# Performance work log

Measured on AMD Instinct MI355X. Metric: run time of the kernel, lower is better.

Reference implementation:

```python
import jax, jax.numpy as jnp
import numpy as np

LAYERS = 2      # LightGCN propagation layers
LAMB = 0.5      # aux loss weight
REG = 1e-4      # embedding reg weight
N_AUX = 2       # len(behaviors) - 1


def setup_inputs() -> dict:
    key = jax.random.key(0)
    k = jax.random.split(key, 8)
    n_users, n_items, d = 100000, 50000, 32
    E = 1000000
    user_emb = (jax.random.normal(k[0], (n_users + 1, d), jnp.float32) * 0.1).at[0].set(0.0)
    item_emb = (jax.random.normal(k[1], (n_items + 1, d), jnp.float32) * 0.1).at[0].set(0.0)
    aux_u = jax.random.randint(k[2], (N_AUX, E), 1, n_users + 1)
    aux_i = jax.random.randint(k[3], (N_AUX, E), 1, n_items + 1)
    aux_edges = jnp.stack([aux_u, aux_i], axis=-1).astype(jnp.int32)
    tgt_u = jax.random.randint(k[4], (E,), 1, n_users + 1)
    tgt_i = jax.random.randint(k[5], (E,), 1, n_items + 1)
    target_edges = jnp.stack([tgt_u, tgt_i], axis=-1).astype(jnp.int32)
    # [B, 1+N_AUX, 3]: per row (user, pos_item, neg_item) for target then each aux behavior
    batch_data = jax.random.randint(k[6], (4096, 1 + N_AUX, 3), 1, n_items + 1).astype(jnp.int32)
    return {"user_emb": user_emb, "item_emb": item_emb, "batch_data": batch_data,
            "aux_edges": aux_edges, "target_edges": target_edges}


def _graph(edges, n_user_rows, N):
    """Symmetric-normalized bipartite LightGCN graph as directed COO (src, dst, w)."""
    u = edges[:, 0]
    v = edges[:, 1] + n_user_rows  # shift item ids into joint node space
    ones = jnp.ones(u.shape[0], jnp.float32)
    deg = jax.ops.segment_sum(ones, u, num_segments=N) + jax.ops.segment_sum(ones, v, num_segments=N)
    dinv = jnp.where(deg > 0, jax.lax.rsqrt(jnp.maximum(deg, 1.0)), 0.0)
    w = dinv[u] * dinv[v]
    src = jnp.concatenate([u, v])
    dst = jnp.concatenate([v, u])
    w2 = jnp.concatenate([w, w])
    return src, dst, w2


def _lightgcn(emb, src, dst, w, N):
    """L-layer LightGCN propagation, mean over layers 0..L."""
    acc = emb
    cur = emb
    for _ in range(LAYERS):
        cur = jax.ops.segment_sum(w[:, None] * cur[src], dst, num_segments=N)
        acc = acc + cur
    return acc / (LAYERS + 1)


def _prob(ue, ie, u, i):
    return jax.nn.relu(jnp.sum(ue[u] * ie[i], axis=-1))


def _bpr(p, n):
    return -jnp.mean(jax.nn.log_sigmoid(p - n))


def reference(user_emb, item_emb, batch_data, aux_edges, target_edges):
    Nu = user_emb.shape[0]
    N = Nu + item_emb.shape[0]
    all_emb = jnp.concatenate([user_emb, item_emb], axis=0)
    tgt_g = _graph(target_edges, Nu, N)

    user, p_item, n_item = batch_data[:, 0, 0], batch_data[:, 0, 1], batch_data[:, 0, 2]
    aux_user, aux_p, aux_n = batch_data[:, 1:, 0], batch_data[:, 1:, 1], batch_data[:, 1:, 2]

    cps, cns, dps, dns, aps, ans, aux_losses = [], [], [], [], [], [], []
    for idx in range(N_AUX):
        # combine graph = aux behavior edges union target edges
        comb_edges = jnp.concatenate([aux_edges[idx], target_edges], axis=0)
        ce = _lightgcn(all_emb, *_graph(comb_edges, Nu, N), N)
        cu, ci = ce[:Nu], ce[Nu:]
        cps.append(_prob(cu, ci, user, p_item))
        cns.append(_prob(cu, ci, user, n_item))

        ae = _lightgcn(all_emb, *_graph(aux_edges[idx], Nu, N), N)
        au, ai = ae[:Nu], ae[Nu:]
        aps.append(_prob(au, ai, user, p_item))
        ans.append(_prob(au, ai, user, n_item))

        # condition: propagate aux embeddings through the target graph
        de = _lightgcn(ae, *tgt_g, N)
        du, di = de[:Nu], de[Nu:]
        dps.append(_prob(du, di, user, p_item))
        dns.append(_prob(du, di, user, n_item))

        ps = jnp.sum(au[aux_user[:, idx]] * ai[aux_p[:, idx]], axis=-1)
        ns = jnp.sum(au[aux_user[:, idx]] * ai[aux_n[:, idx]], axis=-1)
        aux_losses.append(_bpr(ps, ns))

    aux_loss = jnp.mean(jnp.stack(aux_losses))

    def front_door(cond, comb, aux):
        return jnp.sum(cond * jnp.sum(comb * aux, axis=0), axis=0)

    p_scores = front_door(jnp.stack(dps), jnp.stack(cps), jnp.stack(aps))
    n_scores = front_door(jnp.stack(dns), jnp.stack(cns), jnp.stack(ans))
    rec_loss = _bpr(p_scores, n_scores)
    emb_loss = (jnp.linalg.norm(user_emb) + jnp.linalg.norm(item_emb)) / item_emb.shape[0]
    return rec_loss + LAMB * aux_loss + REG * emb_loss
```

## Files before the change

### kernel.cpp

```cpp
#include <hip/hip_runtime.h>
#include <math.h>

#define D 32
#define ROWU 16
#define NBK 1024
#define BSHIFT 8
#define TILE_H 16384
#define TILE_BIN 2048
#define BCAP 7680

typedef unsigned int u32;
typedef unsigned short u16;

__device__ __forceinline__ float logsigf(float x) {
  return fminf(x, 0.f) - log1pf(expf(-fabsf(x)));
}

__device__ __forceinline__ float lo16(u32 u) { return __uint_as_float(u << 16); }
__device__ __forceinline__ float hi16(u32 u) { return __uint_as_float(u & 0xFFFF0000u); }
__device__ __forceinline__ u32 pk2(float a, float b) {
  u32 ua = __float_as_uint(a), ub = __float_as_uint(b);
  u32 ra = (ua + 0x7FFFu + ((ua >> 16) & 1u)) >> 16;
  u32 rb = (ub + 0x7FFFu + ((ub >> 16) & 1u)) >> 16;
  return (ra & 0xFFFFu) | (rb << 16);
}
__device__ __forceinline__ float bfat(const u16* __restrict__ p, size_t off) {
  return __uint_as_float(((u32)p[off]) << 16);
}
__device__ __forceinline__ void accum8(float* a, float w, uint4 x) {
  a[0] += w * lo16(x.x); a[1] += w * hi16(x.x);
  a[2] += w * lo16(x.y); a[3] += w * hi16(x.y);
  a[4] += w * lo16(x.z); a[5] += w * hi16(x.z);
  a[6] += w * lo16(x.w); a[7] += w * hi16(x.w);
}
__device__ __forceinline__ uint4 pack8(const float* a, float w) {
  return make_uint4(pk2(w * a[0], w * a[1]), pk2(w * a[2], w * a[3]),
                    pk2(w * a[4], w * a[5]), pk2(w * a[6], w * a[7]));
}


__global__ void hist_kernel(const int2* __restrict__ tgt, const int2* __restrict__ aux,
                            int E, int Nu, int BPS, int* __restrict__ bcur) {
  __shared__ int lh[NBK];
  int seg = blockIdx.x / BPS;
  int blk = blockIdx.x - seg * BPS;
  const int2* edges = (seg == 0) ? tgt : aux + (size_t)(seg - 1) * E;
  for (int b = threadIdx.x; b < NBK; b += 256) lh[b] = 0;
  __syncthreads();
  int e0 = blk * TILE_H;
  for (int k = threadIdx.x; k < TILE_H; k += 256) {
    int e = e0 + k;
    if (e < E) {
      int2 ed = edges[e];
      atomicAdd(&lh[ed.x >> BSHIFT], 1);
      atomicAdd(&lh[(ed.y + Nu) >> BSHIFT], 1);
    }
  }
  __syncthreads();
  for (int b = threadIdx.x; b < NBK; b += 256)
    if (lh[b]) atomicAdd(&bcur[seg * NBK + b], lh[b]);
}

__global__ void bscan_kernel(int* __restrict__ bcur) {
  int* b = bcur + blockIdx.x * NBK;
  int lane = threadIdx.x;
  int carry = 0;
  for (int base = 0; base < NBK; base += 64) {
    int i = base + lane;
    int v = b[i];
    int s = v;
    #pragma unroll
    for (int o = 1; o < 64; o <<= 1) {
      int t = __shfl_up(s, o);
      if (lane >= o) s += t;
    }
    b[i] = carry + s - v;
    carry += __shfl(s, 63);
  }
}

__global__ void bin_kernel(const int2* __restrict__ tgt, const int2* __restrict__ aux,
                           int E, int Nu, int BPS, int* __restrict__ bcur,
                           int* __restrict__ binned) {
  __shared__ int stage[2 * TILE_BIN];
  __shared__ int lh[NBK];
  __shared__ int loff[NBK];
  __shared__ int gb[NBK];
  __shared__ int wred[4];
  __shared__ int stot;
  int seg = blockIdx.x / BPS;
  int blk = blockIdx.x - seg * BPS;
  const int2* edges = (seg == 0) ? tgt : aux + (size_t)(seg - 1) * E;
  int* out = binned + (size_t)seg * 2 * E;
  int tid = threadIdx.x;
  for (int b = tid; b < NBK; b += 256) lh[b] = 0;
  __syncthreads();
  int e0 = blk * TILE_BIN;
  int pkv[16];
  int pb[16];
  int pr[16];
  #pragma unroll
  for (int it = 0; it < 8; ++it) {
    int e = e0 + tid + it * 256;
    bool ok = e < E;
    int2 ed = ok ? edges[e] : make_int2(0, -Nu);
    int u = ed.x, v = ed.y + Nu;
    int b1 = u >> BSHIFT, b2 = v >> BSHIFT;
    pkv[2 * it] = ((u & 255) << 18) | v;
    pb[2 * it] = b1;
    pr[2 * it] = ok ? atomicAdd(&lh[b1], 1) : 0;
    pkv[2 * it + 1] = ((v & 255) << 18) | u;
    pb[2 * it + 1] = b2;
    pr[2 * it + 1] = ok ? atomicAdd(&lh[b2], 1) : 0;
  }
  __syncthreads();
  int lane = tid & 63, wid = tid >> 6;
  int b4 = tid * 4;
  int v0 = lh[b4], v1 = lh[b4 + 1], v2 = lh[b4 + 2], v3 = lh[b4 + 3];
  int tsum = v0 + v1 + v2 + v3;
  int incl = tsum;
  #pragma unroll
  for (int o = 1; o < 64; o <<= 1) {
    int t = __shfl_up(incl, o);
    if (lane >= o) incl += t;
  }
  if (lane == 63) wred[wid] = incl;
  __syncthreads();
  int wbase = 0;
  for (int w = 0; w < wid; ++w) wbase += wred[w];
  int excl = wbase + incl - tsum;
  loff[b4] = excl;
  loff[b4 + 1] = excl + v0;
  loff[b4 + 2] = excl + v0 + v1;
  loff[b4 + 3] = excl + v0 + v1 + v2;
  if (tid == 255) stot = excl + tsum;
  #pragma unroll
  for (int j = 0; j < 4; ++j) {
    int b = b4 + j;
    int c = lh[b];
    gb[b] = c ? atomicAdd(&bcur[seg * NBK + b], c) : 0;
  }
  __syncthreads();
  #pragma unroll
  for (int it = 0; it < 16; ++it) {
    int e = e0 + tid + (it >> 1) * 256;
    if (e < E) stage[loff[pb[it]] + pr[it]] = pkv[it];
  }
  __syncthreads();
  int tot = stot;
  for (int k = tid; k < tot; k += 256) {
    int lo = 0, hi = NBK;
    while (lo < hi) {
      int mid = (lo + hi) >> 1;
      if (loff[mid] <= k) lo = mid + 1; else hi = mid;
    }
    int b = lo - 1;
    out[gb[b] + (k - loff[b])] = stage[k];
  }
}

__global__ void bucket_csr_kernel(const int* __restrict__ binned,
                                  const int* __restrict__ bend, int E2, int N, int NBKe,
                                  int* __restrict__ deg3, int* __restrict__ rp3,
                                  int* __restrict__ col_all) {
  __shared__ int ent[BCAP];
  __shared__ int cnt[256];
  __shared__ int off[256];
  __shared__ int wred[4];
  int seg = blockIdx.x / NBKe;
  int bkt = blockIdx.x - seg * NBKe;
  int node0 = bkt << BSHIFT;
  const int* bc = bend + seg * NBK;
  int start = (bkt == 0) ? 0 : bc[bkt - 1];
  int end = bc[bkt];
  int cntE = end - start;
  const int* src = binned + (size_t)seg * E2 + start;
  bool inLds = (cntE <= BCAP);
  if (inLds)
    for (int k = threadIdx.x; k < cntE; k += 256) ent[k] = src[k];
  cnt[threadIdx.x] = 0;
  __syncthreads();
  for (int k = threadIdx.x; k < cntE; k += 256) {
    int en = inLds ? ent[k] : src[k];
    atomicAdd(&cnt[en >> 18], 1);
  }
  __syncthreads();
  int lane = threadIdx.x & 63, wid = threadIdx.x >> 6;
  int v = cnt[threadIdx.x];
  int incl = v;
  #pragma unroll
  for (int o = 1; o < 64; o <<= 1) {
    int t = __shfl_up(incl, o);
    if (lane >= o) incl += t;
  }
  if (lane == 63) wred[wid] = incl;
  __syncthreads();
  int wbase = 0;
  for (int w = 0; w < wid; ++w) wbase += wred[w];
  off[threadIdx.x] = wbase + incl - v;
  int node = node0 + (int)threadIdx.x;
  if (node < N) {
    deg3[(size_t)seg * N + node] = v;
    rp3[(size_t)seg * (N + 1) + node] = start + wbase + incl - v;
  }
  if (bkt == 0 && threadIdx.x == 0) rp3[(size_t)seg * (N + 1) + N] = E2;
  __syncthreads();
  cnt[threadIdx.x] = 0;
  __syncthreads();
  int* col = col_all + (size_t)seg * E2 + start;
  for (int k = threadIdx.x; k < cntE; k += 256) {
    int en = inLds ? ent[k] : src[k];
    int lb = en >> 18;
    int pos = atomicAdd(&cnt[lb], 1);
    col[off[lb] + pos] = en & 0x3FFFF;
  }
}

__global__ void dinv_all_kernel(const int* __restrict__ deg3, float* __restrict__ dinv5,
                                int N) {
  int n = blockIdx.x * blockDim.x + threadIdx.x;
  if (n >= N) return;
  int dt = deg3[n], d0 = deg3[N + n], d1 = deg3[2 * N + n];
  dinv5[n]         = dt ? rsqrtf((float)dt) : 0.f;
  dinv5[N + n]     = d0 ? rsqrtf((float)d0) : 0.f;
  dinv5[2 * N + n] = d1 ? rsqrtf((float)d1) : 0.f;
  int c0 = dt + d0, c1 = dt + d1;
  dinv5[3 * N + n] = c0 ? rsqrtf((float)c0) : 0.f;
  dinv5[4 * N + n] = c1 ? rsqrtf((float)c1) : 0.f;
}

__global__ void cvt_emb_kernel(const float2* __restrict__ ue, long nu2,
                               const float2* __restrict__ ie, long ni2,
                               u32* __restrict__ emb) {
  long i = (long)blockIdx.x * blockDim.x + threadIdx.x;
  if (i >= nu2 + ni2) return;
  float2 v = (i < nu2) ? ue[i] : ie[i - nu2];
  emb[i] = pk2(v.x, v.y);
}


__global__ void gather_fused_all_kernel(const int* __restrict__ rp3,
                                        const int* __restrict__ col_all,
                                        const float* __restrict__ dinv5,
                                        const uint4* __restrict__ emb,
                                        uint4* __restrict__ BaAll, uint4* __restrict__ BcAll,
                                        int N, int E2) {
  const int* rpA0 = rp3 + (size_t)1 * (N + 1);
  const int* rpA1 = rp3 + (size_t)2 * (N + 1);
  const int* colA0 = col_all + (size_t)1 * E2;
  const int* colA1 = col_all + (size_t)2 * E2;
  const float* dvA0 = dinv5 + (size_t)1 * N;
  const float* dvA1 = dinv5 + (size_t)2 * N;
  const float* dvC0 = dinv5 + (size_t)3 * N;
  const float* dvC1 = dinv5 + (size_t)4 * N;
  int t = blockIdx.x * blockDim.x + threadIdx.x;
  int n = t >> 2;
  if (n >= N) return;
  int lane = t & 3;
  float aA0[8] = {0, 0, 0, 0, 0, 0, 0, 0};
  float aA1[8] = {0, 0, 0, 0, 0, 0, 0, 0};
  float aC0[8] = {0, 0, 0, 0, 0, 0, 0, 0};
  float aC1[8] = {0, 0, 0, 0, 0, 0, 0, 0};
  int s = rpA0[n], e = rpA0[n + 1];
  int j = s;
  for (; j + 1 < e; j += 2) {
    int c0 = colA0[j], c1 = colA0[j + 1];
    float wa0 = dvA0[c0], wc0 = dvC0[c0];
    float wa1 = dvA0[c1], wc1 = dvC0[c1];
    uint4 x0 = emb[(size_t)c0 * 4 + lane];
    uint4 x1 = emb[(size_t)c1 * 4 + lane];
    accum8(aA0, wa0, x0); accum8(aC0, wc0, x0);
    accum8(aA0, wa1, x1); accum8(aC0, wc1, x1);
  }
  if (j < e) {
    int c = colA0[j];
    float wa = dvA0[c], wc = dvC0[c];
    uint4 x = emb[(size_t)c * 4 + lane];
    accum8(aA0, wa, x); accum8(aC0, wc, x);
  }
  s = rpA1[n]; e = rpA1[n + 1];
  j = s;
  for (; j + 1 < e; j += 2) {
    int c0 = colA1[j], c1 = colA1[j + 1];
    float wa0 = dvA1[c0], wc0 = dvC1[c0];
    float wa1 = dvA1[c1], wc1 = dvC1[c1];
    uint4 x0 = emb[(size_t)c0 * 4 + lane];
    uint4 x1 = emb[(size_t)c1 * 4 + lane];
    accum8(aA1, wa0, x0); accum8(aC1, wc0, x0);
    accum8(aA1, wa1, x1); accum8(aC1, wc1, x1);
  }
  if (j < e) {
    int c = colA1[j];
    float wa = dvA1[c], wc = dvC1[c];
    uint4 x = emb[(size_t)c * 4 + lane];
    accum8(aA1, wa, x); accum8(aC1, wc, x);
  }
  s = rp3[n]; e = rp3[n + 1];
  j = s;
  for (; j + 1 < e; j += 2) {
    int c0 = col_all[j], c1 = col_all[j + 1];
    float w00 = dvC0[c0], w10 = dvC1[c0];
    float w01 = dvC0[c1], w11 = dvC1[c1];
    uint4 x0 = emb[(size_t)c0 * 4 + lane];
    uint4 x1 = emb[(size_t)c1 * 4 + lane];
    accum8(aC0, w00, x0); accum8(aC1, w10, x0);
    accum8(aC0, w01, x1); accum8(aC1, w11, x1);
  }
  if (j < e) {
    int c = col_all[j];
    float w0 = dvC0[c], w1 = dvC1[c];
    uint4 x = emb[(size_t)c * 4 + lane];
    accum8(aC0, w0, x); accum8(aC1, w1, x);
  }
  size_t o = (size_t)n * 4 + lane;
  size_t rowN4 = (size_t)N * 4;
  BaAll[o] = pack8(aA0, dvA0[n]);
  BaAll[rowN4 + o] = pack8(aA1, dvA1[n]);
  BcAll[o] = pack8(aC0, dvC0[n]);
  BcAll[rowN4 + o] = pack8(aC1, dvC1[n]);
}

__global__ void gather_avg_kernel(const int* __restrict__ rp3, const int* __restrict__ col_all,
                                  const float* __restrict__ dinv5,
                                  const uint4* __restrict__ emb,
                                  const uint4* __restrict__ BaAll, uint4* __restrict__ AI,
                                  int N, int E2) {
  int idx = blockIdx.y;
  const int* rp = rp3 + (size_t)(1 + idx) * (N + 1);
  const int* col = col_all + (size_t)(1 + idx) * E2;
  const float* dv = dinv5 + (size_t)(1 + idx) * N;
  const uint4* cur = BaAll + (size_t)idx * N * 4;
  int t = blockIdx.x * blockDim.x + threadIdx.x;
  int n = t >> 2;
  if (n >= N) return;
  int lane = t & 3;
  float acc[8] = {0, 0, 0, 0, 0, 0, 0, 0};
  int s = rp[n], e = rp[n + 1];
  int j = s;
  for (; j + 3 < e; j += 4) {
    int c0 = col[j], c1 = col[j + 1], c2 = col[j + 2], c3 = col[j + 3];
    float w0 = dv[c0], w1 = dv[c1], w2 = dv[c2], w3 = dv[c3];
    uint4 x0 = cur[(size_t)c0 * 4 + lane];
    uint4 x1 = cur[(size_t)c1 * 4 + lane];
    uint4 x2 = cur[(size_t)c2 * 4 + lane];
    uint4 x3 = cur[(size_t)c3 * 4 + lane];
    accum8(acc, w0, x0);
    accum8(acc, w1, x1);
    accum8(acc, w2, x2);
    accum8(acc, w3, x3);
  }
  for (; j < e; ++j) {
    int c = col[j];
    float w = dv[c];
    uint4 x = cur[(size_t)c * 4 + lane];
    accum8(acc, w, x);
  }
  float wn = dv[n];
  uint4 e4 = emb[(size_t)n * 4 + lane];
  uint4 b4 = cur[(size_t)n * 4 + lane];
  float r[8];
  r[0] = (lo16(e4.x) + lo16(b4.x) + wn * acc[0]) * (1.f / 3.f);
  r[1] = (hi16(e4.x) + hi16(b4.x) + wn * acc[1]) * (1.f / 3.f);
  r[2] = (lo16(e4.y) + lo16(b4.y) + wn * acc[2]) * (1.f / 3.f);
  r[3] = (hi16(e4.y) + hi16(b4.y) + wn * acc[3]) * (1.f / 3.f);
  r[4] = (lo16(e4.z) + lo16(b4.z) + wn * acc[4]) * (1.f / 3.f);
  r[5] = (hi16(e4.z) + hi16(b4.z) + wn * acc[5]) * (1.f / 3.f);
  r[6] = (lo16(e4.w) + lo16(b4.w) + wn * acc[6]) * (1.f / 3.f);
  r[7] = (hi16(e4.w) + hi16(b4.w) + wn * acc[7]) * (1.f / 3.f);
  AI[(size_t)n * 8 + idx * 4 + lane] = pack8(r, 1.f);
}

__global__ void de_gather_kernel(const int* __restrict__ rp3, const int* __restrict__ col_all,
                                 const float* __restrict__ dinv5,
                                 const uint4* __restrict__ AI, uint4* __restrict__ DeI,
                                 int N) {
  int t = blockIdx.x * blockDim.x + threadIdx.x;
  int n = t >> 3;
  if (n >= N) return;
  int lane = t & 7;
  float acc[8] = {0, 0, 0, 0, 0, 0, 0, 0};
  int s = rp3[n], e = rp3[n + 1];
  int j = s;
  for (; j + 1 < e; j += 2) {
    int c0 = col_all[j], c1 = col_all[j + 1];
    float w0 = dinv5[c0], w1 = dinv5[c1];
    uint4 x0 = AI[(size_t)c0 * 8 + lane];
    uint4 x1 = AI[(size_t)c1 * 8 + lane];
    accum8(acc, w0, x0);
    accum8(acc, w1, x1);
  }
  if (j < e) {
    int c = col_all[j];
    float w = dinv5[c];
    uint4 x = AI[(size_t)c * 8 + lane];
    accum8(acc, w, x);
  }
  DeI[(size_t)n * 8 + lane] = pack8(acc, dinv5[n]);
}


__device__ __forceinline__ float fdim2(const int* __restrict__ rpA, const int* __restrict__ colA,
                                       const int* __restrict__ rpT, const int* __restrict__ colT,
                                       const float* __restrict__ dv,
                                       const u16* __restrict__ base, const u16* __restrict__ L1,
                                       int r, int d) {
  float acc = 0.f;
  for (int j = rpA[r]; j < rpA[r + 1]; ++j) {
    int c = colA[j];
    acc += dv[c] * bfat(L1, (size_t)c * D + d);
  }
  for (int j = rpT[r]; j < rpT[r + 1]; ++j) {
    int c = colT[j];
    acc += dv[c] * bfat(L1, (size_t)c * D + d);
  }
  return (bfat(base, (size_t)r * D + d) + bfat(L1, (size_t)r * D + d) + dv[r] * acc) * (1.f / 3.f);
}

__device__ __forceinline__ float fdim1i(const int* __restrict__ rp, const int* __restrict__ col,
                                        const float* __restrict__ dv,
                                        const u16* __restrict__ base, const u16* __restrict__ L1,
                                        int r, int di) {
  float acc = 0.f;
  for (int j = rp[r]; j < rp[r + 1]; ++j) {
    int c = col[j];
    acc += dv[c] * bfat(L1, (size_t)c * 64 + di);
  }
  return (bfat(base, (size_t)r * 64 + di) + bfat(L1, (size_t)r * 64 + di) + dv[r] * acc) * (1.f / 3.f);
}

__global__ void ce_sparse_kernel(const int* __restrict__ rp3, const int* __restrict__ col_all,
                                 const float* __restrict__ dinv5,
                                 const u32* __restrict__ EMBu, const u32* __restrict__ BcAll,
                                 const int* __restrict__ batch, int Bsz, int Nu, int N, int E2,
                                 float* __restrict__ cps, float* __restrict__ cns) {
  int idx = blockIdx.y;
  const int* rpA = rp3 + (size_t)(1 + idx) * (N + 1);
  const int* colA = col_all + (size_t)(1 + idx) * E2;
  const float* dv = dinv5 + (size_t)(3 + idx) * N;
  const u16* base = (const u16*)EMBu;
  const u16* L1 = (const u16*)(BcAll + (size_t)idx * N * ROWU);
  float* outp = cps + (size_t)idx * Bsz;
  float* outn = cns + (size_t)idx * Bsz;
  int t = blockIdx.x * blockDim.x + threadIdx.x;
  int b = t >> 5, d = t & 31;
  if (b >= Bsz) return;
  int u = batch[b * 9 + 0];
  int p = batch[b * 9 + 1] + Nu;
  int n = batch[b * 9 + 2] + Nu;
  float uv = fdim2(rpA, colA, rp3, col_all, dv, base, L1, u, d);
  float pv = fdim2(rpA, colA, rp3, col_all, dv, base, L1, p, d);
  float nv = fdim2(rpA, colA, rp3, col_all, dv, base, L1, n, d);
  float sp = uv * pv, sn = uv * nv;
  #pragma unroll
  for (int o = 16; o > 0; o >>= 1) {
    sp += __shfl_down(sp, o, 32);
    sn += __shfl_down(sn, o, 32);
  }
  if (d == 0) {
    outp[b] = fmaxf(sp, 0.f);
    outn[b] = fmaxf(sn, 0.f);
  }
}

__global__ void de_sparse_kernel(const int* __restrict__ rp3, const int* __restrict__ col_all,
                                 const float* __restrict__ dinv5,
                                 const u32* __restrict__ AI, const u32* __restrict__ DeI,
                                 const int* __restrict__ batch, int Bsz, int Nu, int N,
                                 float* __restrict__ dps, float* __restrict__ dns) {
  int idx = blockIdx.y;
  const u16* base = (const u16*)AI;
  const u16* L1 = (const u16*)DeI;
  float* outp = dps + (size_t)idx * Bsz;
  float* outn = dns + (size_t)idx * Bsz;
  int t = blockIdx.x * blockDim.x + threadIdx.x;
  int b = t >> 5, d = t & 31;
  if (b >= Bsz) return;
  int di = idx * 32 + d;
  int u = batch[b * 9 + 0];
  int p = batch[b * 9 + 1] + Nu;
  int n = batch[b * 9 + 2] + Nu;
  float uv = fdim1i(rp3, col_all, dinv5, base, L1, u, di);
  float pv = fdim1i(rp3, col_all, dinv5, base, L1, p, di);
  float nv = fdim1i(rp3, col_all, dinv5, base, L1, n, di);
  float sp = uv * pv, sn = uv * nv;
  #pragma unroll
  for (int o = 16; o > 0; o >>= 1) {
    sp += __shfl_down(sp, o, 32);
    sn += __shfl_down(sn, o, 32);
  }
  if (d == 0) {
    outp[b] = fmaxf(sp, 0.f);
    outn[b] = fmaxf(sn, 0.f);
  }
}


__device__ __forceinline__ float dotrow(const u32* __restrict__ a, const u32* __restrict__ b) {
  float s = 0.f;
  #pragma unroll
  for (int k = 0; k < ROWU; ++k) {
    u32 x = a[k], y = b[k];
    s += lo16(x) * lo16(y) + hi16(x) * hi16(y);
  }
  return s;
}

__global__ void score_aux_kernel(const u32* __restrict__ AI, const int* __restrict__ batch,
                                 int Bsz, int Nu, int N, float* __restrict__ aps,
                                 float* __restrict__ ans_, float* __restrict__ accs) {
  int idx = blockIdx.y;
  const u32* A = AI + (size_t)idx * ROWU;
  float* outp = aps + (size_t)idx * Bsz;
  float* outn = ans_ + (size_t)idx * Bsz;
  int b = blockIdx.x * blockDim.x + threadIdx.x;
  float l = 0.f;
  if (b < Bsz) {
    int u = batch[b * 9 + 0];
    int p = batch[b * 9 + 1] + Nu;
    int n = batch[b * 9 + 2] + Nu;
    const u32* ur = A + (size_t)u * 32;
    outp[b] = fmaxf(dotrow(ur, A + (size_t)p * 32), 0.f);
    outn[b] = fmaxf(dotrow(ur, A + (size_t)n * 32), 0.f);
    const int* r = batch + b * 9 + 3 * (1 + idx);
    const u32* aur = A + (size_t)r[0] * 32;
    float ps = dotrow(aur, A + (size_t)(r[1] + Nu) * 32);
    float ns = dotrow(aur, A + (size_t)(r[2] + Nu) * 32);
    l = -logsigf(ps - ns);
  }
  for (int o = 32; o > 0; o >>= 1) l += __shfl_down(l, o);
  if ((threadIdx.x & 63) == 0) atomicAdd(&accs[idx], l);
}

__global__ void recloss_kernel(const float* __restrict__ cps, const float* __restrict__ cns,
                               const float* __restrict__ aps, const float* __restrict__ ans_,
                               const float* __restrict__ dps, const float* __restrict__ dns,
                               int Bsz, int NA, float* __restrict__ acc) {
  int b = blockIdx.x * blockDim.x + threadIdx.x;
  float l = 0.f;
  if (b < Bsz) {
    float dp = 0.f, dn = 0.f, cap = 0.f, can = 0.f;
    for (int i = 0; i < NA; ++i) {
      dp += dps[i * Bsz + b];
      dn += dns[i * Bsz + b];
      cap += cps[i * Bsz + b] * aps[i * Bsz + b];
      can += cns[i * Bsz + b] * ans_[i * Bsz + b];
    }
    l = -logsigf(dp * cap - dn * can);
  }
  for (int o = 32; o > 0; o >>= 1) l += __shfl_down(l, o);
  if ((threadIdx.x & 63) == 0) atomicAdd(acc, l);
}

__global__ void sumsq2_kernel(const float4* __restrict__ xu, int n4u,
                              const float4* __restrict__ xi, int n4i,
                              float* __restrict__ accU, float* __restrict__ accI) {
  __shared__ float redU[4], redI[4];
  int tid = threadIdx.x;
  int gid = blockIdx.x * blockDim.x + tid;
  int stride = gridDim.x * blockDim.x;
  float su = 0.f, si = 0.f;
  for (int i = gid; i < n4u; i += stride) {
    float4 v = xu[i];
    su += v.x * v.x + v.y * v.y + v.z * v.z + v.w * v.w;
  }
  for (int i = gid; i < n4i; i += stride) {
    float4 v = xi[i];
    si += v.x * v.x + v.y * v.y + v.z * v.z + v.w * v.w;
  }
  for (int o = 32; o > 0; o >>= 1) {
    su += __shfl_down(su, o);
    si += __shfl_down(si, o);
  }
  if ((tid & 63) == 0) { redU[tid >> 6] = su; redI[tid >> 6] = si; }
  __syncthreads();
  if (tid == 0) {
    atomicAdd(accU, redU[0] + redU[1] + redU[2] + redU[3]);
    atomicAdd(accI, redI[0] + redI[1] + redI[2] + redI[3]);
  }
}

__global__ void final_kernel(const float* __restrict__ accs, int Bsz, int NA, int NiRows,
                             float* __restrict__ out) {
  float rec = accs[NA] / (float)Bsz;
  float aux = 0.f;
  for (int i = 0; i < NA; ++i) aux += accs[i] / (float)Bsz;
  aux /= (float)NA;
  float embl = (sqrtf(accs[NA + 1]) + sqrtf(accs[NA + 2])) / (float)NiRows;
  out[0] = rec + 0.5f * aux + 1e-4f * embl;
}

extern "C" void kernel_launch(void* const* d_in, const int* in_sizes, int n_in,
                              void* d_out, int out_size, void* d_ws, size_t ws_size,
                              hipStream_t stream) {
  const float* user_emb = (const float*)d_in[0];
  const float* item_emb = (const float*)d_in[1];
  const int* batch = (const int*)d_in[2];
  const int* aux_edges = (const int*)d_in[3];
  const int* tgt_edges = (const int*)d_in[4];

  const int NuRows = in_sizes[0] / D;
  const int NiRows = in_sizes[1] / D;
  const int Bsz = in_sizes[2] / 9;
  const int E = in_sizes[4] / 2;
  const int NA = in_sizes[3] / (2 * E);
  const int N = NuRows + NiRows;
  const int E2 = 2 * E;
  const size_t rowH = (size_t)N * ROWU;
  const int BPS_H = (E + TILE_H - 1) / TILE_H;
  const int BPS_B = (E + TILE_BIN - 1) / TILE_BIN;
  const int NBKe = (N + (1 << BSHIFT) - 1) >> BSHIFT;

  u32* EMBu = (u32*)d_ws;
  u32* AI = EMBu + rowH;
  u32* BaAll = AI + 2 * rowH;
  u32* BcAll = BaAll + 2 * rowH;
  int* deg3 = (int*)(BcAll + 2 * rowH);
  float* dinv5 = (float*)(deg3 + 3 * (size_t)N);
  int* rp3 = (int*)(dinv5 + 5 * (size_t)N);
  int* bcur = rp3 + 3 * (size_t)(N + 1);
  int* col_all = bcur + 3 * (size_t)NBK;
  float* cps = (float*)(col_all + 3 * (size_t)E2);
  float* cns = cps + (size_t)NA * Bsz;
  float* aps = cns + (size_t)NA * Bsz;
  float* ans_ = aps + (size_t)NA * Bsz;
  float* dps = ans_ + (size_t)NA * Bsz;
  float* dns = dps + (size_t)NA * Bsz;
  float* accs = dns + (size_t)NA * Bsz;
  int* binned = (int*)AI;

  const int TB = 256;
  const int gN = (N + TB - 1) / TB;
  const int gN4 = (N * 4 + TB - 1) / TB;
  const int gN8 = (N * 8 + TB - 1) / TB;
  const int gB = (Bsz + TB - 1) / TB;
  const int gB32 = (Bsz * 32 + TB - 1) / TB;
  const long nu2 = (long)NuRows * ROWU;
  const long ni2 = (long)NiRows * ROWU;
  const int gCvt = (int)((nu2 + ni2 + TB - 1) / TB);

  cvt_emb_kernel<<<gCvt, TB, 0, stream>>>((const float2*)user_emb, nu2,
                                          (const float2*)item_emb, ni2, EMBu);

  hipMemsetAsync(bcur, 0, 3 * (size_t)NBK * sizeof(int), stream);
  hist_kernel<<<3 * BPS_H, TB, 0, stream>>>((const int2*)tgt_edges, (const int2*)aux_edges,
                                            E, NuRows, BPS_H, bcur);
  bscan_kernel<<<3, 64, 0, stream>>>(bcur);
  bin_kernel<<<3 * BPS_B, TB, 0, stream>>>((const int2*)tgt_edges, (const int2*)aux_edges,
                                           E, NuRows, BPS_B, bcur, binned);
  bucket_csr_kernel<<<3 * NBKe, TB, 0, stream>>>(binned, bcur, E2, N, NBKe,
                                                 deg3, rp3, col_all);
  dinv_all_kernel<<<gN, TB, 0, stream>>>(deg3, dinv5, N);

  hipMemsetAsync(accs, 0, (size_t)(NA + 3) * sizeof(float), stream);

  dim3 gridG(gN4, NA), gridB(gB, NA), gridS(gB32, NA);

  gather_fused_all_kernel<<<gN4, TB, 0, stream>>>(rp3, col_all, dinv5, (const uint4*)EMBu,
                                                  (uint4*)BaAll, (uint4*)BcAll, N, E2);
  gather_avg_kernel<<<gridG, TB, 0, stream>>>(rp3, col_all, dinv5, (const uint4*)EMBu,
                                              (const uint4*)BaAll, (uint4*)AI, N, E2);
  score_aux_kernel<<<gridB, TB, 0, stream>>>(AI, batch, Bsz, NuRows, N, aps, ans_, accs);
  ce_sparse_kernel<<<gridS, TB, 0, stream>>>(rp3, col_all, dinv5, EMBu, BcAll,
                                             batch, Bsz, NuRows, N, E2, cps, cns);
  de_gather_kernel<<<gN8, TB, 0, stream>>>(rp3, col_all, dinv5, (const uint4*)AI,
                                           (uint4*)BaAll, N);
  de_sparse_kernel<<<gridS, TB, 0, stream>>>(rp3, col_all, dinv5, AI, BaAll,
                                             batch, Bsz, NuRows, N, dps, dns);

  sumsq2_kernel<<<104, TB, 0, stream>>>((const float4*)user_emb,
                                        (int)((size_t)NuRows * D / 4),
                                        (const float4*)item_emb,
                                        (int)((size_t)NiRows * D / 4),
                                        accs + NA + 1, accs + NA + 2);
  recloss_kernel<<<gB, TB, 0, stream>>>(cps, cns, aps, ans_, dps, dns, Bsz, NA, accs + NA);
  final_kernel<<<1, 1, 0, stream>>>(accs, Bsz, NA, NiRows, (float*)d_out);
}
```

Baseline: 651.1 us.

## Split CSR neighbor lists into column-range chunks for cache-local gathers

The CSR build now sorts each node's neighbors by column range (chunks of 2^15 nodes) and records the chunk boundaries in a new mids array. The gather kernels then loop over the chunks in the same order, so every node visits the same region of the embedding table at roughly the same time. The aim is better L2 locality for the random row gathers. In exchange there is more shared-memory and atomic work in bucket_csr, extra boundary loads and loop overhead per node, and more workspace. Threads can also drift apart, so the intended locality is only approximate.

Result: slower. 675.2 us (+3.7%).

```diff
diff --git a/kernel.cpp b/kernel.cpp
--- a/kernel.cpp
+++ b/kernel.cpp
@@ -8,6 +8,8 @@
 #define TILE_H 16384
 #define TILE_BIN 2048
 #define BCAP 7680
+#define RSH 15
+#define MAXR 8
 
 typedef unsigned int u32;
 typedef unsigned short u16;
@@ -36,6 +38,14 @@
 __device__ __forceinline__ uint4 pack8(const float* a, float w) {
   return make_uint4(pk2(w * a[0], w * a[1]), pk2(w * a[2], w * a[3]),
                     pk2(w * a[4], w * a[5]), pk2(w * a[6], w * a[7]));
+}
+
+__device__ __forceinline__ int2 rbounds(const int* __restrict__ rp,
+                                        const int* __restrict__ mids,
+                                        size_t segN, int n, int r, int nr) {
+  int b0 = (r == 0) ? rp[n] : mids[(segN + n) * (MAXR - 1) + (r - 1)];
+  int b1 = (r == nr - 1) ? rp[n + 1] : mids[(segN + n) * (MAXR - 1) + r];
+  return make_int2(b0, b1);
 }
 
 
@@ -161,11 +171,11 @@
 
 __global__ void bucket_csr_kernel(const int* __restrict__ binned,
                                   const int* __restrict__ bend, int E2, int N, int NBKe,
-                                  int* __restrict__ deg3, int* __restrict__ rp3,
-                                  int* __restrict__ col_all) {
+                                  int nr, int* __restrict__ deg3, int* __restrict__ rp3,
+                                  int* __restrict__ mids, int* __restrict__ col_all) {
   __shared__ int ent[BCAP];
-  __shared__ int cnt[256];
-  __shared__ int off[256];
+  __shared__ int cnt[256 * MAXR];
+  __shared__ int off[256 * MAXR];
   __shared__ int wred[4];
   int seg = blockIdx.x / NBKe;
   int bkt = blockIdx.x - seg * NBKe;
@@ -178,16 +188,18 @@
   bool inLds = (cntE <= BCAP);
   if (inLds)
     for (int k = threadIdx.x; k < cntE; k += 256) ent[k] = src[k];
-  cnt[threadIdx.x] = 0;
+  for (int k = threadIdx.x; k < 256 * nr; k += 256) cnt[k] = 0;
   __syncthreads();
   for (int k = threadIdx.x; k < cntE; k += 256) {
     int en = inLds ? ent[k] : src[k];
-    atomicAdd(&cnt[en >> 18], 1);
+    int key = (en >> 18) * nr + ((en & 0x3FFFF) >> RSH);
+    atomicAdd(&cnt[key], 1);
   }
   __syncthreads();
   int lane = threadIdx.x & 63, wid = threadIdx.x >> 6;
-  int v = cnt[threadIdx.x];
-  int incl = v;
+  int tot = 0;
+  for (int r = 0; r < nr; ++r) tot += cnt[threadIdx.x * nr + r];
+  int incl = tot;
   #pragma unroll
   for (int o = 1; o < 64; o <<= 1) {
     int t = __shfl_up(incl, o);
@@ -197,22 +209,34 @@
   __syncthreads();
   int wbase = 0;
   for (int w = 0; w < wid; ++w) wbase += wred[w];
-  off[threadIdx.x] = wbase + incl - v;
+  int excl = wbase + incl - tot;
+  int run = excl;
+  for (int r = 0; r < nr; ++r) {
+    off[threadIdx.x * nr + r] = run;
+    run += cnt[threadIdx.x * nr + r];
+  }
   int node = node0 + (int)threadIdx.x;
   if (node < N) {
-    deg3[(size_t)seg * N + node] = v;
-    rp3[(size_t)seg * (N + 1) + node] = start + wbase + incl - v;
+    deg3[(size_t)seg * N + node] = tot;
+    rp3[(size_t)seg * (N + 1) + node] = start + excl;
+    int* m = mids + ((size_t)seg * N + node) * (MAXR - 1);
+    int acc = excl;
+    for (int r = 1; r < nr; ++r) {
+      acc += cnt[threadIdx.x * nr + r - 1];
+      m[r - 1] = start + acc;
+    }
   }
   if (bkt == 0 && threadIdx.x == 0) rp3[(size_t)seg * (N + 1) + N] = E2;
   __syncthreads();
-  cnt[threadIdx.x] = 0;
+  for (int k = threadIdx.x; k < 256 * nr; k += 256) cnt[k] = 0;
   __syncthreads();
   int* col = col_all + (size_t)seg * E2 + start;
   for (int k = threadIdx.x; k < cntE; k += 256) {
     int en = inLds ? ent[k] : src[k];
-    int lb = en >> 18;
-    int pos = atomicAdd(&cnt[lb], 1);
-    col[off[lb] + pos] = en & 0x3FFFF;
+    int s_ = en & 0x3FFFF;
+    int key = (en >> 18) * nr + (s_ >> RSH);
+    int pos = atomicAdd(&cnt[key], 1);
+    col[off[key] + pos] = s_;
   }
 }
 
@@ -241,10 +265,11 @@
 
 __global__ void gather_fused_all_kernel(const int* __restrict__ rp3,
                                         const int* __restrict__ col_all,
+                                        const int* __restrict__ mids,
                                         const float* __restrict__ dinv5,
                                         const uint4* __restrict__ emb,
                                         uint4* __restrict__ BaAll, uint4* __restrict__ BcAll,
-                                        int N, int E2) {
+                                        int N, int E2, int nr) {
   const int* rpA0 = rp3 + (size_t)1 * (N + 1);
   const int* rpA1 = rp3 + (size_t)2 * (N + 1);
   const int* colA0 = col_all + (size_t)1 * E2;
@@ -261,56 +286,58 @@
   float aA1[8] = {0, 0, 0, 0, 0, 0, 0, 0};
   float aC0[8] = {0, 0, 0, 0, 0, 0, 0, 0};
   float aC1[8] = {0, 0, 0, 0, 0, 0, 0, 0};
-  int s = rpA0[n], e = rpA0[n + 1];
-  int j = s;
-  for (; j + 1 < e; j += 2) {
-    int c0 = colA0[j], c1 = colA0[j + 1];
-    float wa0 = dvA0[c0], wc0 = dvC0[c0];
-    float wa1 = dvA0[c1], wc1 = dvC0[c1];
-    uint4 x0 = emb[(size_t)c0 * 4 + lane];
-    uint4 x1 = emb[(size_t)c1 * 4 + lane];
-    accum8(aA0, wa0, x0); accum8(aC0, wc0, x0);
-    accum8(aA0, wa1, x1); accum8(aC0, wc1, x1);
-  }
-  if (j < e) {
-    int c = colA0[j];
-    float wa = dvA0[c], wc = dvC0[c];
-    uint4 x = emb[(size_t)c * 4 + lane];
-    accum8(aA0, wa, x); accum8(aC0, wc, x);
-  }
-  s = rpA1[n]; e = rpA1[n + 1];
-  j = s;
-  for (; j + 1 < e; j += 2) {
-    int c0 = colA1[j], c1 = colA1[j + 1];
-    float wa0 = dvA1[c0], wc0 = dvC1[c0];
-    float wa1 = dvA1[c1], wc1 = dvC1[c1];
-    uint4 x0 = emb[(size_t)c0 * 4 + lane];
-    uint4 x1 = emb[(size_t)c1 * 4 + lane];
-    accum8(aA1, wa0, x0); accum8(aC1, wc0, x0);
-    accum8(aA1, wa1, x1); accum8(aC1, wc1, x1);
-  }
-  if (j < e) {
-    int c = colA1[j];
-    float wa = dvA1[c], wc = dvC1[c];
-    uint4 x = emb[(size_t)c * 4 + lane];
-    accum8(aA1, wa, x); accum8(aC1, wc, x);
-  }
-  s = rp3[n]; e = rp3[n + 1];
-  j = s;
-  for (; j + 1 < e; j += 2) {
-    int c0 = col_all[j], c1 = col_all[j + 1];
-    float w00 = dvC0[c0], w10 = dvC1[c0];
-    float w01 = dvC0[c1], w11 = dvC1[c1];
-    uint4 x0 = emb[(size_t)c0 * 4 + lane];
-    uint4 x1 = emb[(size_t)c1 * 4 + lane];
-    accum8(aC0, w00, x0); accum8(aC1, w10, x0);
-    accum8(aC0, w01, x1); accum8(aC1, w11, x1);
-  }
-  if (j < e) {
-    int c = col_all[j];
-    float w0 = dvC0[c], w1 = dvC1[c];
-    uint4 x = emb[(size_t)c * 4 + lane];
-    accum8(aC0, w0, x); accum8(aC1, w1, x);
+  for (int r = 0; r < nr; ++r) {
+    int2 b = rbounds(rpA0, mids, (size_t)1 * N, n, r, nr);
+    int j = b.x;
+    for (; j + 1 < b.y; j += 2) {
+      int c0 = colA0[j], c1 = colA0[j + 1];
+      float wa0 = dvA0[c0], wc0 = dvC0[c0];
+      float wa1 = dvA0[c1], wc1 = dvC0[c1];
+      uint4 x0 = emb[(size_t)c0 * 4 + lane];
+      uint4 x1 = emb[(size_t)c1 * 4 + lane];
+      accum8(aA0, wa0, x0); accum8(aC0, wc0, x0);
+      accum8(aA0, wa1, x1); accum8(aC0, wc1, x1);
+    }
+    if (j < b.y) {
+      int c = colA0[j];
+      float wa = dvA0[c], wc = dvC0[c];
+      uint4 x = emb[(size_t)c * 4 + lane];
+      accum8(aA0, wa, x); accum8(aC0, wc, x);
+    }
+    b = rbounds(rpA1, mids, (size_t)2 * N, n, r, nr);
+    j = b.x;
+    for (; j + 1 < b.y; j += 2) {
+      int c0 = colA1[j], c1 = colA1[j + 1];
+      float wa0 = dvA1[c0], wc0 = dvC1[c0];
+      float wa1 = dvA1[c1], wc1 = dvC1[c1];
+      uint4 x0 = emb[(size_t)c0 * 4 + lane];
+      uint4 x1 = emb[(size_t)c1 * 4 + lane];
+      accum8(aA1, wa0, x0); accum8(aC1, wc0, x0);
+      accum8(aA1, wa1, x1); accum8(aC1, wc1, x1);
+    }
+    if (j < b.y) {
+      int c = colA1[j];
+      float wa = dvA1[c], wc = dvC1[c];
+      uint4 x = emb[(size_t)c * 4 + lane];
+      accum8(aA1, wa, x); accum8(aC1, wc, x);
+    }
+    b = rbounds(rp3, mids, 0, n, r, nr);
+    j = b.x;
+    for (; j + 1 < b.y; j += 2) {
+      int c0 = col_all[j], c1 = col_all[j + 1];
+      float w00 = dvC0[c0], w10 = dvC1[c0];
+      float w01 = dvC0[c1], w11 = dvC1[c1];
+      uint4 x0 = emb[(size_t)c0 * 4 + lane];
+      uint4 x1 = emb[(size_t)c1 * 4 + lane];
+      accum8(aC0, w00, x0); accum8(aC1, w10, x0);
+      accum8(aC0, w01, x1); accum8(aC1, w11, x1);
+    }
+    if (j < b.y) {
+      int c = col_all[j];
+      float w0 = dvC0[c], w1 = dvC1[c];
+      uint4 x = emb[(size_t)c * 4 + lane];
+      accum8(aC0, w0, x); accum8(aC1, w1, x);
+    }
   }
   size_t o = (size_t)n * 4 + lane;
   size_t rowN4 = (size_t)N * 4;
@@ -321,79 +348,86 @@
 }
 
 __global__ void gather_avg_kernel(const int* __restrict__ rp3, const int* __restrict__ col_all,
+                                  const int* __restrict__ mids,
                                   const float* __restrict__ dinv5,
                                   const uint4* __restrict__ emb,
                                   const uint4* __restrict__ BaAll, uint4* __restrict__ AI,
-                                  int N, int E2) {
+                                  int N, int E2, int nr) {
   int idx = blockIdx.y;
   const int* rp = rp3 + (size_t)(1 + idx) * (N + 1);
   const int* col = col_all + (size_t)(1 + idx) * E2;
   const float* dv = dinv5 + (size_t)(1 + idx) * N;
   const uint4* cur = BaAll + (size_t)idx * N * 4;
+  size_t segN = (size_t)(1 + idx) * N;
   int t = blockIdx.x * blockDim.x + threadIdx.x;
   int n = t >> 2;
   if (n >= N) return;
   int lane = t & 3;
   float acc[8] = {0, 0, 0, 0, 0, 0, 0, 0};
-  int s = rp[n], e = rp[n + 1];
-  int j = s;
-  for (; j + 3 < e; j += 4) {
-    int c0 = col[j], c1 = col[j + 1], c2 = col[j + 2], c3 = col[j + 3];
-    float w0 = dv[c0], w1 = dv[c1], w2 = dv[c2], w3 = dv[c3];
-    uint4 x0 = cur[(size_t)c0 * 4 + lane];
-    uint4 x1 = cur[(size_t)c1 * 4 + lane];
-    uint4 x2 = cur[(size_t)c2 * 4 + lane];
-    uint4 x3 = cur[(size_t)c3 * 4 + lane];
-    accum8(acc, w0, x0);
-    accum8(acc, w1, x1);
-    accum8(acc, w2, x2);
-    accum8(acc, w3, x3);
-  }
-  for (; j < e; ++j) {
-    int c = col[j];
-    float w = dv[c];
-    uint4 x = cur[(size_t)c * 4 + lane];
-    accum8(acc, w, x);
+  for (int r = 0; r < nr; ++r) {
+    int2 bb = rbounds(rp, mids, segN, n, r, nr);
+    int j = bb.x;
+    for (; j + 3 < bb.y; j += 4) {
+      int c0 = col[j], c1 = col[j + 1], c2 = col[j + 2], c3 = col[j + 3];
+      float w0 = dv[c0], w1 = dv[c1], w2 = dv[c2], w3 = dv[c3];
+      uint4 x0 = cur[(size_t)c0 * 4 + lane];
+      uint4 x1 = cur[(size_t)c1 * 4 + lane];
+      uint4 x2 = cur[(size_t)c2 * 4 + lane];
+      uint4 x3 = cur[(size_t)c3 * 4 + lane];
+      accum8(acc, w0, x0);
+      accum8(acc, w1, x1);
+      accum8(acc, w2, x2);
+      accum8(acc, w3, x3);
+    }
+    for (; j < bb.y; ++j) {
+      int c = col[j];
+      float w = dv[c];
+      uint4 x = cur[(size_t)c * 4 + lane];
+      accum8(acc, w, x);
+    }
   }
   float wn = dv[n];
   uint4 e4 = emb[(size_t)n * 4 + lane];
   uint4 b4 = cur[(size_t)n * 4 + lane];
-  float r[8];
-  r[0] = (lo16(e4.x) + lo16(b4.x) + wn * acc[0]) * (1.f / 3.f);
-  r[1] = (hi16(e4.x) + hi16(b4.x) + wn * acc[1]) * (1.f / 3.f);
-  r[2] = (lo16(e4.y) + lo16(b4.y) + wn * acc[2]) * (1.f / 3.f);
-  r[3] = (hi16(e4.y) + hi16(b4.y) + wn * acc[3]) * (1.f / 3.f);
-  r[4] = (lo16(e4.z) + lo16(b4.z) + wn * acc[4]) * (1.f / 3.f);
-  r[5] = (hi16(e4.z) + hi16(b4.z) + wn * acc[5]) * (1.f / 3.f);
-  r[6] = (lo16(e4.w) + lo16(b4.w) + wn * acc[6]) * (1.f / 3.f);
-  r[7] = (hi16(e4.w) + hi16(b4.w) + wn * acc[7]) * (1.f / 3.f);
-  AI[(size_t)n * 8 + idx * 4 + lane] = pack8(r, 1.f);
+  float r8[8];
+  r8[0] = (lo16(e4.x) + lo16(b4.x) + wn * acc[0]) * (1.f / 3.f);
+  r8[1] = (hi16(e4.x) + hi16(b4.x) + wn * acc[1]) * (1.f / 3.f);
+  r8[2] = (lo16(e4.y) + lo16(b4.y) + wn * acc[2]) * (1.f / 3.f);
+  r8[3] = (hi16(e4.y) + hi16(b4.y) + wn * acc[3]) * (1.f / 3.f);
+  r8[4] = (lo16(e4.z) + lo16(b4.z) + wn * acc[4]) * (1.f / 3.f);
+  r8[5] = (hi16(e4.z) + hi16(b4.z) + wn * acc[5]) * (1.f / 3.f);
+  r8[6] = (lo16(e4.w) + lo16(b4.w) + wn * acc[6]) * (1.f / 3.f);
+  r8[7] = (hi16(e4.w) + hi16(b4.w) + wn * acc[7]) * (1.f / 3.f);
+  AI[(size_t)n * 8 + idx * 4 + lane] = pack8(r8, 1.f);
 }
 
 __global__ void de_gather_kernel(const int* __restrict__ rp3, const int* __restrict__ col_all,
+                                 const int* __restrict__ mids,
                                  const float* __restrict__ dinv5,
                                  const uint4* __restrict__ AI, uint4* __restrict__ DeI,
-                                 int N) {
+                                 int N, int nr) {
   int t = blockIdx.x * blockDim.x + threadIdx.x;
   int n = t >> 3;
   if (n >= N) return;
   int lane = t & 7;
   float acc[8] = {0, 0, 0, 0, 0, 0, 0, 0};
-  int s = rp3[n], e = rp3[n + 1];
-  int j = s;
-  for (; j + 1 < e; j += 2) {
-    int c0 = col_all[j], c1 = col_all[j + 1];
-    float w0 = dinv5[c0], w1 = dinv5[c1];
-    uint4 x0 = AI[(size_t)c0 * 8 + lane];
-    uint4 x1 = AI[(size_t)c1 * 8 + lane];
-    accum8(acc, w0, x0);
-    accum8(acc, w1, x1);
-  }
-  if (j < e) {
-    int c = col_all[j];
-    float w = dinv5[c];
-    uint4 x = AI[(size_t)c * 8 + lane];
-    accum8(acc, w, x);
+  for (int r = 0; r < nr; ++r) {
+    int2 b = rbounds(rp3, mids, 0, n, r, nr);
+    int j = b.x;
+    for (; j + 1 < b.y; j += 2) {
+      int c0 = col_all[j], c1 = col_all[j + 1];
+      float w0 = dinv5[c0], w1 = dinv5[c1];
+      uint4 x0 = AI[(size_t)c0 * 8 + lane];
+      uint4 x1 = AI[(size_t)c1 * 8 + lane];
+      accum8(acc, w0, x0);
+      accum8(acc, w1, x1);
+    }
+    if (j < b.y) {
+      int c = col_all[j];
+      float w = dinv5[c];
+      uint4 x = AI[(size_t)c * 8 + lane];
+      accum8(acc, w, x);
+    }
   }
   DeI[(size_t)n * 8 + lane] = pack8(acc, dinv5[n]);
 }
@@ -609,6 +643,7 @@
   const int BPS_H = (E + TILE_H - 1) / TILE_H;
   const int BPS_B = (E + TILE_BIN - 1) / TILE_BIN;
   const int NBKe = (N + (1 << BSHIFT) - 1) >> BSHIFT;
+  const int nr = ((N - 1) >> RSH) + 1;
 
   u32* EMBu = (u32*)d_ws;
   u32* AI = EMBu + rowH;
@@ -619,7 +654,8 @@
   int* rp3 = (int*)(dinv5 + 5 * (size_t)N);
   int* bcur = rp3 + 3 * (size_t)(N + 1);
   int* col_all = bcur + 3 * (size_t)NBK;
-  float* cps = (float*)(col_all + 3 * (size_t)E2);
+  int* mids = col_all + 3 * (size_t)E2;
+  float* cps = (float*)(mids + 3 * (size_t)N * (MAXR - 1));
   float* cns = cps + (size_t)NA * Bsz;
   float* aps = cns + (size_t)NA * Bsz;
   float* ans_ = aps + (size_t)NA * Bsz;
@@ -647,23 +683,24 @@
   bscan_kernel<<<3, 64, 0, stream>>>(bcur);
   bin_kernel<<<3 * BPS_B, TB, 0, stream>>>((const int2*)tgt_edges, (const int2*)aux_edges,
                                            E, NuRows, BPS_B, bcur, binned);
-  bucket_csr_kernel<<<3 * NBKe, TB, 0, stream>>>(binned, bcur, E2, N, NBKe,
-                                                 deg3, rp3, col_all);
+  bucket_csr_kernel<<<3 * NBKe, TB, 0, stream>>>(binned, bcur, E2, N, NBKe, nr,
+                                                 deg3, rp3, mids, col_all);
   dinv_all_kernel<<<gN, TB, 0, stream>>>(deg3, dinv5, N);
 
   hipMemsetAsync(accs, 0, (size_t)(NA + 3) * sizeof(float), stream);
 
   dim3 gridG(gN4, NA), gridB(gB, NA), gridS(gB32, NA);
 
-  gather_fused_all_kernel<<<gN4, TB, 0, stream>>>(rp3, col_all, dinv5, (const uint4*)EMBu,
-                                                  (uint4*)BaAll, (uint4*)BcAll, N, E2);
-  gather_avg_kernel<<<gridG, TB, 0, stream>>>(rp3, col_all, dinv5, (const uint4*)EMBu,
-                                              (const uint4*)BaAll, (uint4*)AI, N, E2);
+  gather_fused_all_kernel<<<gN4, TB, 0, stream>>>(rp3, col_all, mids, dinv5,
+                                                  (const uint4*)EMBu,
+                                                  (uint4*)BaAll, (uint4*)BcAll, N, E2, nr);
+  gather_avg_kernel<<<gridG, TB, 0, stream>>>(rp3, col_all, mids, dinv5, (const uint4*)EMBu,
+                                              (const uint4*)BaAll, (uint4*)AI, N, E2, nr);
   score_aux_kernel<<<gridB, TB, 0, stream>>>(AI, batch, Bsz, NuRows, N, aps, ans_, accs);
   ce_sparse_kernel<<<gridS, TB, 0, stream>>>(rp3, col_all, dinv5, EMBu, BcAll,
                                              batch, Bsz, NuRows, N, E2, cps, cns);
-  de_gather_kernel<<<gN8, TB, 0, stream>>>(rp3, col_all, dinv5, (const uint4*)AI,
-                                           (uint4*)BaAll, N);
+  de_gather_kernel<<<gN8, TB, 0, stream>>>(rp3, col_all, mids, dinv5, (const uint4*)AI,
+                                           (uint4*)BaAll, N, nr);
   de_sparse_kernel<<<gridS, TB, 0, stream>>>(rp3, col_all, dinv5, AI, BaAll,
                                              batch, Bsz, NuRows, N, dps, dns);
 
```
